# Kernel optimization log

Hardware: AMD Instinct MI355X
Metric: run time of the kernel (lower is better)

Reference implementation:

```python
import jax, jax.numpy as jnp
import numpy as np

B, N, C = 4, 6144, 256
M = 3
n = N // M  # nodes per modality (contiguous blocks)


def setup_inputs() -> dict:
    key = jax.random.key(0)
    ks = jax.random.split(key, 12)
    s = 1.0 / np.sqrt(C)
    sb = 1.0 / np.sqrt(3 * C)
    return {
        "distribution_edge": jax.random.normal(ks[0], (B, N, N), jnp.float32),
        "feature_node": jax.random.normal(ks[1], (B, N, C), jnp.float32),
        "modal_id": jnp.broadcast_to(jnp.repeat(jnp.arange(M, dtype=jnp.int32), n), (B, N)),
        # per-modality params, stacked on leading axis of size M=3
        "W_feat": jax.random.normal(ks[2], (M, C, C), jnp.float32) * s,
        "b_feat": jax.random.normal(ks[3], (M, C), jnp.float32) * s,
        "W_raw": jax.random.normal(ks[4], (M, C, C), jnp.float32) * s,
        "b_raw": jax.random.normal(ks[5], (M, C), jnp.float32) * s,
        "W_beta": jax.random.normal(ks[6], (M, 3 * C), jnp.float32) * sb,
        "b_beta": jax.random.normal(ks[7], (M,), jnp.float32) * sb,
        "ln_gamma": jnp.ones((M, C), jnp.float32),
        "ln_beta": jnp.zeros((M, C), jnp.float32),
    }


def reference(distribution_edge, feature_node, modal_id, W_feat, b_feat,
              W_raw, b_raw, W_beta, b_beta, ln_gamma, ln_beta):
    EPS_L1, EPS_LN = 1e-12, 1e-5  # torch F.normalize / LayerNorm defaults
    diag_mask = 1.0 - jnp.eye(n, dtype=distribution_edge.dtype)  # zero self-edges
    outs = []
    for i in range(M):  # fixed small modality loop (structurally distinct params)
        sl = slice(i * n, (i + 1) * n)
        # masked L1 row-normalization of intra-modality edges  [B,n,n]
        e = distribution_edge[:, sl, sl] * diag_mask
        e = e / jnp.maximum(jnp.sum(jnp.abs(e), axis=-1, keepdims=True), EPS_L1)
        x = feature_node[:, sl, :]  # [B,n,C]
        # neighbor aggregation + linear projections
        aggr = jnp.einsum('bij,bjc->bic', e, x) @ W_raw[i] + b_raw[i]
        feat = x @ W_feat[i] + b_feat[i]
        # sigmoid gate over concatenated features -> [B,n,1]
        cat = jnp.concatenate([feat, aggr, feat - aggr], axis=-1)
        beta = jax.nn.sigmoid(cat @ W_beta[i] + b_beta[i])[..., None]
        h = feat * beta + aggr * (1.0 - beta)
        mu = jnp.mean(h, axis=-1, keepdims=True)
        var = jnp.mean((h - mu) ** 2, axis=-1, keepdims=True)
        h = (h - mu) * jax.lax.rsqrt(var + EPS_LN) * ln_gamma[i] + ln_beta[i]
        outs.append(jax.nn.relu(h))
    return jnp.concatenate(outs, axis=1)  # [B,N,C]
```

## Files before the change

### kernel.cpp

```cpp
#include <hip/hip_runtime.h>
#include <cstdint>
#include <cstddef>

#define B_   4
#define N_   6144
#define C_   256
#define M_   3
#define NLOC 2048

static_assert(N_ == M_ * NLOC, "shape");

typedef __bf16 bf16;
typedef __bf16 bf16x8 __attribute__((ext_vector_type(8)));
typedef float  f32x4  __attribute__((ext_vector_type(4)));

__global__ void transpose_k(const float* __restrict__ src, bf16* __restrict__ dst,
                            int R, int Cc) {
    __shared__ bf16 tile[32][33];
    const int s  = blockIdx.z;
    const int rb = blockIdx.y * 32, cb = blockIdx.x * 32;
    const float* sp = src + (size_t)s * R * Cc;
    bf16*        dp = dst + (size_t)s * R * Cc;
    const int tx = threadIdx.x, ty = threadIdx.y;
#pragma unroll
    for (int i = 0; i < 4; ++i)
        tile[ty + 8 * i][tx] = (bf16)sp[(size_t)(rb + ty + 8 * i) * Cc + (cb + tx)];
    __syncthreads();
#pragma unroll
    for (int i = 0; i < 4; ++i)
        dp[(size_t)(cb + ty + 8 * i) * R + (rb + tx)] = tile[tx][ty + 8 * i];
}

__global__ __launch_bounds__(256) void aggr_gemm_k(
    const float* __restrict__ e,
    const bf16* __restrict__ xT,
    bf16* __restrict__ aggr)
{
    __shared__ __align__(16) bf16 Abuf[64 * 32];
    __shared__ __align__(16) bf16 Bbuf[256 * 32];
    __shared__ float rsum[256];

    const int rt = blockIdx.x, i = blockIdx.y, b = blockIdx.z;
    const int t = threadIdx.x;
    const int w = t >> 6, lane = t & 63, l15 = lane & 15, quad = lane >> 4;

    const int r_stage = t >> 2;
    const int ch8 = (t & 3) * 8;

    const int diag_local = rt * 64 + r_stage;
    const float* eptr = e + ((size_t)(b * N_ + i * NLOC + rt * 64 + r_stage)) * N_
                          + i * NLOC + ch8;
    const bf16* xTbase = xT + (size_t)(b * C_) * N_ + i * NLOC + ch8;

    f32x4 acc[4][4];
#pragma unroll
    for (int mt = 0; mt < 4; ++mt)
#pragma unroll
        for (int nt = 0; nt < 4; ++nt) { f32x4 z = {0.f, 0.f, 0.f, 0.f}; acc[mt][nt] = z; }

    float psum = 0.f;

    for (int kk = 0; kk < NLOC; kk += 32) {
        __syncthreads();
        f32x4 v0 = *(const f32x4*)(const void*)(eptr + kk);
        f32x4 v1 = *(const f32x4*)(const void*)(eptr + kk + 4);
        float vals[8] = {v0[0], v0[1], v0[2], v0[3], v1[0], v1[1], v1[2], v1[3]};
        const int d = diag_local - kk - ch8;
        if ((unsigned)d < 8u) vals[d] = 0.f;
        bf16x8 ab;
#pragma unroll
        for (int j = 0; j < 8; ++j) {
            const bf16 h = (bf16)vals[j];
            ab[j] = h;
            psum += fabsf((float)h);
        }
        *(bf16x8*)(void*)&Abuf[r_stage * 32 + ch8] = ab;
#pragma unroll
        for (int q = 0; q < 4; ++q) {
            const int c = q * 64 + r_stage;
            f32x4 v = *(const f32x4*)(const void*)(xTbase + (size_t)c * N_ + kk);
            *(f32x4*)(void*)&Bbuf[c * 32 + ch8] = v;
        }
        __syncthreads();
        bf16x8 af[4];
#pragma unroll
        for (int mt = 0; mt < 4; ++mt)
            af[mt] = *(const bf16x8*)(const void*)&Abuf[(mt * 16 + l15) * 32 + quad * 8];
#pragma unroll
        for (int nt = 0; nt < 4; ++nt) {
            bf16x8 bv = *(const bf16x8*)(const void*)&Bbuf[(w * 64 + nt * 16 + l15) * 32 + quad * 8];
#pragma unroll
            for (int mt = 0; mt < 4; ++mt)
                acc[mt][nt] = __builtin_amdgcn_mfma_f32_16x16x32_bf16(af[mt], bv, acc[mt][nt], 0, 0, 0);
        }
    }

    rsum[t] = psum;
    __syncthreads();

#pragma unroll
    for (int mt = 0; mt < 4; ++mt) {
#pragma unroll
        for (int reg = 0; reg < 4; ++reg) {
            const int rr = mt * 16 + quad * 4 + reg;
            const float s = rsum[rr * 4] + rsum[rr * 4 + 1] + rsum[rr * 4 + 2] + rsum[rr * 4 + 3];
            const float inv = 1.f / fmaxf(s, 1e-12f);
            bf16* op = aggr + ((size_t)(b * N_ + i * NLOC + rt * 64 + rr)) * C_;
#pragma unroll
            for (int nt = 0; nt < 4; ++nt) {
                const int c = w * 64 + nt * 16 + l15;
                op[c] = (bf16)(acc[mt][nt][reg] * inv);
            }
        }
    }
}

__global__ __launch_bounds__(256) void node_final_k(
    const float* __restrict__ x,
    const bf16* __restrict__ aggr,
    const bf16* __restrict__ WfT,
    const bf16* __restrict__ WrT,
    const float* __restrict__ b_feat,
    const float* __restrict__ b_raw,
    const float* __restrict__ W_beta,
    const float* __restrict__ b_beta,
    const float* __restrict__ ln_g,
    const float* __restrict__ ln_b,
    float* __restrict__ out)
{
    __shared__ __align__(16) bf16 Ax[64 * 32], Ag[64 * 32];
    __shared__ __align__(16) bf16 Bf[256 * 32], Br[256 * 32];
    __shared__ float pbf[256], pbr[256], pwA[256], pwB[256], pgm[256], plb[256];

    const int rt = blockIdx.x, i = blockIdx.y, b = blockIdx.z;
    const int t = threadIdx.x;
    const int w = t >> 6, lane = t & 63, l15 = lane & 15, quad = lane >> 4;

    {
        const int c = t;
        const float w3 = W_beta[i * 768 + 512 + c];
        pbf[c] = b_feat[i * C_ + c];
        pbr[c] = b_raw[i * C_ + c];
        pwA[c] = W_beta[i * 768 + c] + w3;
        pwB[c] = W_beta[i * 768 + 256 + c] - w3;
        pgm[c] = ln_g[i * C_ + c];
        plb[c] = ln_b[i * C_ + c];
    }

    f32x4 accf[16], accg[16];
#pragma unroll
    for (int nt = 0; nt < 16; ++nt) { f32x4 z = {0.f, 0.f, 0.f, 0.f}; accf[nt] = z; accg[nt] = z; }

    const int r_stage = t >> 2;
    const int ch8 = (t & 3) * 8;
    const size_t nodeRow = (size_t)(b * N_ + i * NLOC + rt * 64 + r_stage);
    const float* xp = x   + nodeRow * C_ + ch8;
    const bf16* gp = aggr + nodeRow * C_ + ch8;
    const bf16* wf = WfT + (size_t)(i * C_) * C_ + ch8;
    const bf16* wr = WrT + (size_t)(i * C_) * C_ + ch8;

    for (int kk = 0; kk < C_; kk += 32) {
        __syncthreads();
        {
            f32x4 v0 = *(const f32x4*)(const void*)(xp + kk);
            f32x4 v1 = *(const f32x4*)(const void*)(xp + kk + 4);
            bf16x8 ax;
#pragma unroll
            for (int j = 0; j < 4; ++j) { ax[j] = (bf16)v0[j]; ax[j + 4] = (bf16)v1[j]; }
            *(bf16x8*)(void*)&Ax[r_stage * 32 + ch8] = ax;
        }
        *(f32x4*)(void*)&Ag[r_stage * 32 + ch8] = *(const f32x4*)(const void*)(gp + kk);
#pragma unroll
        for (int q = 0; q < 4; ++q) {
            const int o = q * 64 + r_stage;
            *(f32x4*)(void*)&Bf[o * 32 + ch8] = *(const f32x4*)(const void*)(wf + (size_t)o * C_ + kk);
            *(f32x4*)(void*)&Br[o * 32 + ch8] = *(const f32x4*)(const void*)(wr + (size_t)o * C_ + kk);
        }
        __syncthreads();
        const bf16x8 ax = *(const bf16x8*)(const void*)&Ax[(w * 16 + l15) * 32 + quad * 8];
        const bf16x8 ag = *(const bf16x8*)(const void*)&Ag[(w * 16 + l15) * 32 + quad * 8];
#pragma unroll
        for (int nt = 0; nt < 16; ++nt) {
            const bf16x8 bfv = *(const bf16x8*)(const void*)&Bf[(nt * 16 + l15) * 32 + quad * 8];
            const bf16x8 brv = *(const bf16x8*)(const void*)&Br[(nt * 16 + l15) * 32 + quad * 8];
            accf[nt] = __builtin_amdgcn_mfma_f32_16x16x32_bf16(ax, bfv, accf[nt], 0, 0, 0);
            accg[nt] = __builtin_amdgcn_mfma_f32_16x16x32_bf16(ag, brv, accg[nt], 0, 0, 0);
        }
    }

    const float bb = b_beta[i];
    const int rowbase = i * NLOC + rt * 64 + w * 16 + quad * 4;
#pragma unroll
    for (int reg = 0; reg < 4; ++reg) {
        float pb = 0.f;
#pragma unroll
        for (int nt = 0; nt < 16; ++nt) {
            const int c = nt * 16 + l15;
            const float f = accf[nt][reg] + pbf[c];
            const float g = accg[nt][reg] + pbr[c];
            pb += f * pwA[c] + g * pwB[c];
        }
#pragma unroll
        for (int off = 1; off < 16; off <<= 1) pb += __shfl_xor(pb, off, 16);
        const float beta = 1.f / (1.f + expf(-(pb + bb)));
        float sh = 0.f, sh2 = 0.f;
#pragma unroll
        for (int nt = 0; nt < 16; ++nt) {
            const int c = nt * 16 + l15;
            const float f = accf[nt][reg] + pbf[c];
            const float g = accg[nt][reg] + pbr[c];
            const float h = g + (f - g) * beta;
            sh += h; sh2 += h * h;
        }
#pragma unroll
        for (int off = 1; off < 16; off <<= 1) {
            sh  += __shfl_xor(sh,  off, 16);
            sh2 += __shfl_xor(sh2, off, 16);
        }
        const float mu   = sh * (1.f / 256.f);
        const float var  = sh2 * (1.f / 256.f) - mu * mu;
        const float rstd = rsqrtf(var + 1e-5f);
        float* op = out + (size_t)(b * N_ + rowbase + reg) * C_;
#pragma unroll
        for (int nt = 0; nt < 16; ++nt) {
            const int c = nt * 16 + l15;
            const float f = accf[nt][reg] + pbf[c];
            const float g = accg[nt][reg] + pbr[c];
            const float h = g + (f - g) * beta;
            const float o = (h - mu) * rstd * pgm[c] + plb[c];
            op[c] = fmaxf(o, 0.f);
        }
    }
}

extern "C" void kernel_launch(void* const* d_in, const int* in_sizes, int n_in,
                              void* d_out, int out_size, void* d_ws, size_t ws_size,
                              hipStream_t stream) {
    const float* e       = (const float*)d_in[0];
    const float* x       = (const float*)d_in[1];
    const float* W_feat  = (const float*)d_in[3];
    const float* b_feat  = (const float*)d_in[4];
    const float* W_raw   = (const float*)d_in[5];
    const float* b_raw   = (const float*)d_in[6];
    const float* W_beta  = (const float*)d_in[7];
    const float* b_beta  = (const float*)d_in[8];
    const float* ln_g    = (const float*)d_in[9];
    const float* ln_b    = (const float*)d_in[10];
    float* out = (float*)d_out;

    char* ws = (char*)d_ws;
    bf16* xT   = (bf16*)(ws);
    bf16* WfT  = (bf16*)(ws + 12582912);
    bf16* WrT  = (bf16*)(ws + 12582912 + 393216);
    bf16* aggr = (bf16*)(ws + 12582912 + 2 * 393216);

    dim3 tb(32, 8);
    transpose_k<<<dim3(C_ / 32, N_ / 32, B_), tb, 0, stream>>>(x, xT, N_, C_);
    transpose_k<<<dim3(C_ / 32, C_ / 32, M_), tb, 0, stream>>>(W_feat, WfT, C_, C_);
    transpose_k<<<dim3(C_ / 32, C_ / 32, M_), tb, 0, stream>>>(W_raw, WrT, C_, C_);

    aggr_gemm_k<<<dim3(NLOC / 64, M_, B_), 256, 0, stream>>>(e, xT, aggr);
    node_final_k<<<dim3(NLOC / 64, M_, B_), 256, 0, stream>>>(
        x, aggr, WfT, WrT, b_feat, b_raw, W_beta, b_beta, ln_g, ln_b, out);
}
```

Measured before the change: 814.8 us.

## Fuse aggregation GEMM with node epilogue, double-buffer loads, merge transposes

The three transpose launches become one kernel, and the aggregation GEMM and node-final kernel become a single kernel. The normalised aggregate now stays in LDS instead of going through a bf16 global buffer. The row tile shrinks from 64 to 32, which doubles the number of blocks, and the edge and xT loads are register double-buffered with split barriers. The cost is that each block re-reads the full W_feat and W_raw tiles per 32 rows, and the LayerNorm needs cross-wave reductions through LDS.

```diff
diff --git a/kernel.cpp b/kernel.cpp
--- a/kernel.cpp
+++ b/kernel.cpp
@@ -7,227 +7,329 @@
 #define C_   256
 #define M_   3
 #define NLOC 2048
+#define R_T  32
 
 static_assert(N_ == M_ * NLOC, "shape");
 
 typedef __bf16 bf16;
+typedef __bf16 bf16x4 __attribute__((ext_vector_type(4)));
 typedef __bf16 bf16x8 __attribute__((ext_vector_type(8)));
 typedef float  f32x4  __attribute__((ext_vector_type(4)));
 
-__global__ void transpose_k(const float* __restrict__ src, bf16* __restrict__ dst,
-                            int R, int Cc) {
+#define BARRIER_LGKM() asm volatile("s_waitcnt lgkmcnt(0)\n\ts_barrier" ::: "memory")
+
+__global__ void transpose_all_k(const float* __restrict__ x,
+                                const float* __restrict__ Wf,
+                                const float* __restrict__ Wr,
+                                bf16* __restrict__ xT,
+                                bf16* __restrict__ WfT,
+                                bf16* __restrict__ WrT) {
+    const int id = blockIdx.x;
+    const float* src;
+    bf16* dst;
+    int R, rb, cb;
+    if (id < 6144) {
+        const int s = id / 1536, r = id % 1536;
+        rb = (r >> 3) * 32; cb = (r & 7) * 32;
+        src = x  + (size_t)s * N_ * C_;
+        dst = xT + (size_t)s * N_ * C_;
+        R = N_;
+    } else {
+        const int id2 = id - 6144;
+        const int mat = id2 / 192, r = id2 % 192;
+        const int s = r / 64, r2 = r % 64;
+        rb = (r2 >> 3) * 32; cb = (r2 & 7) * 32;
+        src = (mat ? Wr : Wf) + (size_t)s * C_ * C_;
+        dst = (mat ? WrT : WfT) + (size_t)s * C_ * C_;
+        R = C_;
+    }
     __shared__ bf16 tile[32][33];
-    const int s  = blockIdx.z;
-    const int rb = blockIdx.y * 32, cb = blockIdx.x * 32;
-    const float* sp = src + (size_t)s * R * Cc;
-    bf16*        dp = dst + (size_t)s * R * Cc;
     const int tx = threadIdx.x, ty = threadIdx.y;
 #pragma unroll
-    for (int i = 0; i < 4; ++i)
-        tile[ty + 8 * i][tx] = (bf16)sp[(size_t)(rb + ty + 8 * i) * Cc + (cb + tx)];
-    __syncthreads();
-#pragma unroll
-    for (int i = 0; i < 4; ++i)
-        dp[(size_t)(cb + ty + 8 * i) * R + (rb + tx)] = tile[tx][ty + 8 * i];
+    for (int k = 0; k < 4; ++k)
+        tile[ty + 8 * k][tx] = (bf16)src[(size_t)(rb + ty + 8 * k) * C_ + (cb + tx)];
+    __syncthreads();
+#pragma unroll
+    for (int k = 0; k < 4; ++k)
+        dst[(size_t)(cb + ty + 8 * k) * R + (rb + tx)] = tile[tx][ty + 8 * k];
 }
 
-__global__ __launch_bounds__(256) void aggr_gemm_k(
+struct P1 {
+    bf16  Abuf[2][4][R_T][8];
+    bf16  Bbuf[2][4][256][8];
+    float rsum[R_T][8];
+};
+struct P2 {
+    bf16  Pg[32][R_T][8];
+    bf16  Bw[4][256][8];
+    float prm[6][256];
+    float red[3][2][R_T];
+    float rinv[R_T];
+};
+union FusedLds { P1 p1; P2 p2; };
+
+__global__ __launch_bounds__(256) void fused_k(
     const float* __restrict__ e,
-    const bf16* __restrict__ xT,
-    bf16* __restrict__ aggr)
+    const float* __restrict__ x,
+    const bf16*  __restrict__ xT,
+    const bf16*  __restrict__ WfT,
+    const bf16*  __restrict__ WrT,
+    const float* __restrict__ b_feat, const float* __restrict__ b_raw,
+    const float* __restrict__ W_beta, const float* __restrict__ b_beta,
+    const float* __restrict__ ln_g,   const float* __restrict__ ln_b,
+    float* __restrict__ out)
 {
-    __shared__ __align__(16) bf16 Abuf[64 * 32];
-    __shared__ __align__(16) bf16 Bbuf[256 * 32];
-    __shared__ float rsum[256];
+    __shared__ FusedLds u;
 
     const int rt = blockIdx.x, i = blockIdx.y, b = blockIdx.z;
     const int t = threadIdx.x;
     const int w = t >> 6, lane = t & 63, l15 = lane & 15, quad = lane >> 4;
-
-    const int r_stage = t >> 2;
-    const int ch8 = (t & 3) * 8;
-
-    const int diag_local = rt * 64 + r_stage;
-    const float* eptr = e + ((size_t)(b * N_ + i * NLOC + rt * 64 + r_stage)) * N_
-                          + i * NLOC + ch8;
-    const bf16* xTbase = xT + (size_t)(b * C_) * N_ + i * NLOC + ch8;
-
-    f32x4 acc[4][4];
-#pragma unroll
-    for (int mt = 0; mt < 4; ++mt)
+    const int R0 = rt * R_T;
+
+    const int ar  = t >> 3;
+    const int ac4 = (t & 7) * 4;
+    const int bc  = t >> 2;
+    const int bch8 = (t & 3) * 8;
+    const int dconst = R0 + ar - ac4;
+
+    const float* eptr = e + ((size_t)(b * N_ + i * NLOC + R0 + ar)) * N_
+                          + i * NLOC + ac4;
+    const bf16* xTb = xT + ((size_t)(b * C_ + bc)) * N_ + i * NLOC + bch8;
+
+    f32x4 acc[2][4];
+#pragma unroll
+    for (int mt = 0; mt < 2; ++mt)
 #pragma unroll
         for (int nt = 0; nt < 4; ++nt) { f32x4 z = {0.f, 0.f, 0.f, 0.f}; acc[mt][nt] = z; }
-
     float psum = 0.f;
 
-    for (int kk = 0; kk < NLOC; kk += 32) {
-        __syncthreads();
-        f32x4 v0 = *(const f32x4*)(const void*)(eptr + kk);
-        f32x4 v1 = *(const f32x4*)(const void*)(eptr + kk + 4);
-        float vals[8] = {v0[0], v0[1], v0[2], v0[3], v1[0], v1[1], v1[2], v1[3]};
-        const int d = diag_local - kk - ch8;
-        if ((unsigned)d < 8u) vals[d] = 0.f;
-        bf16x8 ab;
-#pragma unroll
-        for (int j = 0; j < 8; ++j) {
-            const bf16 h = (bf16)vals[j];
-            ab[j] = h;
-            psum += fabsf((float)h);
-        }
-        *(bf16x8*)(void*)&Abuf[r_stage * 32 + ch8] = ab;
-#pragma unroll
-        for (int q = 0; q < 4; ++q) {
-            const int c = q * 64 + r_stage;
-            f32x4 v = *(const f32x4*)(const void*)(xTbase + (size_t)c * N_ + kk);
-            *(f32x4*)(void*)&Bbuf[c * 32 + ch8] = v;
-        }
-        __syncthreads();
-        bf16x8 af[4];
-#pragma unroll
-        for (int mt = 0; mt < 4; ++mt)
-            af[mt] = *(const bf16x8*)(const void*)&Abuf[(mt * 16 + l15) * 32 + quad * 8];
-#pragma unroll
-        for (int nt = 0; nt < 4; ++nt) {
-            bf16x8 bv = *(const bf16x8*)(const void*)&Bbuf[(w * 64 + nt * 16 + l15) * 32 + quad * 8];
-#pragma unroll
-            for (int mt = 0; mt < 4; ++mt)
-                acc[mt][nt] = __builtin_amdgcn_mfma_f32_16x16x32_bf16(af[mt], bv, acc[mt][nt], 0, 0, 0);
-        }
-    }
-
-    rsum[t] = psum;
-    __syncthreads();
-
-#pragma unroll
-    for (int mt = 0; mt < 4; ++mt) {
-#pragma unroll
-        for (int reg = 0; reg < 4; ++reg) {
-            const int rr = mt * 16 + quad * 4 + reg;
-            const float s = rsum[rr * 4] + rsum[rr * 4 + 1] + rsum[rr * 4 + 2] + rsum[rr * 4 + 3];
-            const float inv = 1.f / fmaxf(s, 1e-12f);
-            bf16* op = aggr + ((size_t)(b * N_ + i * NLOC + rt * 64 + rr)) * C_;
-#pragma unroll
-            for (int nt = 0; nt < 4; ++nt) {
-                const int c = w * 64 + nt * 16 + l15;
-                op[c] = (bf16)(acc[mt][nt][reg] * inv);
-            }
-        }
-    }
-}
-
-__global__ __launch_bounds__(256) void node_final_k(
-    const float* __restrict__ x,
-    const bf16* __restrict__ aggr,
-    const bf16* __restrict__ WfT,
-    const bf16* __restrict__ WrT,
-    const float* __restrict__ b_feat,
-    const float* __restrict__ b_raw,
-    const float* __restrict__ W_beta,
-    const float* __restrict__ b_beta,
-    const float* __restrict__ ln_g,
-    const float* __restrict__ ln_b,
-    float* __restrict__ out)
-{
-    __shared__ __align__(16) bf16 Ax[64 * 32], Ag[64 * 32];
-    __shared__ __align__(16) bf16 Bf[256 * 32], Br[256 * 32];
-    __shared__ float pbf[256], pbr[256], pwA[256], pwB[256], pgm[256], plb[256];
-
-    const int rt = blockIdx.x, i = blockIdx.y, b = blockIdx.z;
-    const int t = threadIdx.x;
-    const int w = t >> 6, lane = t & 63, l15 = lane & 15, quad = lane >> 4;
-
+    f32x4 eA, xA0, xA1, xA2, xA3;
+    f32x4 eB, xB0, xB1, xB2, xB3;
+
+#define AG_LOAD(EV, X0, X1, X2, X3, KK)                                          \
+    do {                                                                         \
+        EV = *(const f32x4*)(const void*)(eptr + (KK));                          \
+        X0 = *(const f32x4*)(const void*)(xTb + (size_t)0   * N_ + (KK));        \
+        X1 = *(const f32x4*)(const void*)(xTb + (size_t)64  * N_ + (KK));        \
+        X2 = *(const f32x4*)(const void*)(xTb + (size_t)128 * N_ + (KK));        \
+        X3 = *(const f32x4*)(const void*)(xTb + (size_t)192 * N_ + (KK));        \
+    } while (0)
+
+#define AG_STAGE(EV, X0, X1, X2, X3, KK, BUF)                                    \
+    do {                                                                         \
+        const int d = dconst - (KK);                                             \
+        bf16x4 a4;                                                               \
+        _Pragma("unroll")                                                        \
+        for (int j = 0; j < 4; ++j) {                                            \
+            float v = (EV)[j];                                                   \
+            v = (d == j) ? 0.f : v;                                              \
+            const bf16 hh = (bf16)v;                                             \
+            a4[j] = hh;                                                          \
+            psum += fabsf((float)hh);                                            \
+        }                                                                        \
+        *(bf16x4*)(void*)&u.p1.Abuf[BUF][ac4 >> 3][ar][ac4 & 7] = a4;            \
+        *(f32x4*)(void*)&u.p1.Bbuf[BUF][t & 3][bc      ][0] = X0;                \
+        *(f32x4*)(void*)&u.p1.Bbuf[BUF][t & 3][bc +  64][0] = X1;                \
+        *(f32x4*)(void*)&u.p1.Bbuf[BUF][t & 3][bc + 128][0] = X2;                \
+        *(f32x4*)(void*)&u.p1.Bbuf[BUF][t & 3][bc + 192][0] = X3;                \
+    } while (0)
+
+#define AG_COMPUTE(BUF)                                                          \
+    do {                                                                         \
+        const bf16x8 af0 = *(const bf16x8*)(const void*)&u.p1.Abuf[BUF][quad][l15][0];      \
+        const bf16x8 af1 = *(const bf16x8*)(const void*)&u.p1.Abuf[BUF][quad][16 + l15][0]; \
+        _Pragma("unroll")                                                        \
+        for (int nt = 0; nt < 4; ++nt) {                                         \
+            const bf16x8 bv = *(const bf16x8*)(const void*)                      \
+                &u.p1.Bbuf[BUF][quad][w * 64 + nt * 16 + l15][0];                \
+            acc[0][nt] = __builtin_amdgcn_mfma_f32_16x16x32_bf16(af0, bv, acc[0][nt], 0, 0, 0); \
+            acc[1][nt] = __builtin_amdgcn_mfma_f32_16x16x32_bf16(af1, bv, acc[1][nt], 0, 0, 0); \
+        }                                                                        \
+    } while (0)
+
+    AG_LOAD(eA, xA0, xA1, xA2, xA3, 0);
+#pragma unroll 1
+    for (int kk = 0; kk < NLOC; kk += 64) {
+        AG_LOAD(eB, xB0, xB1, xB2, xB3, kk + 32);
+        AG_STAGE(eA, xA0, xA1, xA2, xA3, kk, 0);
+        BARRIER_LGKM();
+        if (kk + 64 < NLOC) AG_LOAD(eA, xA0, xA1, xA2, xA3, kk + 64);
+        AG_COMPUTE(0);
+        AG_STAGE(eB, xB0, xB1, xB2, xB3, kk + 32, 1);
+        BARRIER_LGKM();
+        AG_COMPUTE(1);
+    }
+#undef AG_LOAD
+#undef AG_STAGE
+#undef AG_COMPUTE
+
+    u.p1.rsum[ar][t & 7] = psum;
+    __syncthreads();
+    float rs = 0.f;
+    if (t < R_T) {
+#pragma unroll
+        for (int j = 0; j < 8; ++j) rs += u.p1.rsum[t][j];
+    }
+    __syncthreads();
+    if (t < R_T) u.p2.rinv[t] = 1.f / fmaxf(rs, 1e-12f);
     {
         const int c = t;
         const float w3 = W_beta[i * 768 + 512 + c];
-        pbf[c] = b_feat[i * C_ + c];
-        pbr[c] = b_raw[i * C_ + c];
-        pwA[c] = W_beta[i * 768 + c] + w3;
-        pwB[c] = W_beta[i * 768 + 256 + c] - w3;
-        pgm[c] = ln_g[i * C_ + c];
-        plb[c] = ln_b[i * C_ + c];
-    }
-
-    f32x4 accf[16], accg[16];
-#pragma unroll
-    for (int nt = 0; nt < 16; ++nt) { f32x4 z = {0.f, 0.f, 0.f, 0.f}; accf[nt] = z; accg[nt] = z; }
-
-    const int r_stage = t >> 2;
-    const int ch8 = (t & 3) * 8;
-    const size_t nodeRow = (size_t)(b * N_ + i * NLOC + rt * 64 + r_stage);
-    const float* xp = x   + nodeRow * C_ + ch8;
-    const bf16* gp = aggr + nodeRow * C_ + ch8;
-    const bf16* wf = WfT + (size_t)(i * C_) * C_ + ch8;
-    const bf16* wr = WrT + (size_t)(i * C_) * C_ + ch8;
-
+        u.p2.prm[0][c] = b_feat[i * C_ + c];
+        u.p2.prm[1][c] = b_raw[i * C_ + c];
+        u.p2.prm[2][c] = W_beta[i * 768 + c] + w3;
+        u.p2.prm[3][c] = W_beta[i * 768 + 256 + c] - w3;
+        u.p2.prm[4][c] = ln_g[i * C_ + c];
+        u.p2.prm[5][c] = ln_b[i * C_ + c];
+    }
+    __syncthreads();
+#pragma unroll
+    for (int mt = 0; mt < 2; ++mt) {
+#pragma unroll
+        for (int reg = 0; reg < 4; ++reg) {
+            const int r = mt * 16 + quad * 4 + reg;
+            const float iv = u.p2.rinv[r];
+#pragma unroll
+            for (int nt = 0; nt < 4; ++nt) {
+                const int c = w * 64 + nt * 16 + l15;
+                u.p2.Pg[c >> 3][r][c & 7] = (bf16)(acc[mt][nt][reg] * iv);
+            }
+        }
+    }
+    __syncthreads();
+
+    const int rg = w & 1, cg = w >> 1;
+    const int wo = t >> 2;
+    const int wch8 = (t & 3) * 8;
+
+    const float* xrowp = x + ((size_t)(b * N_ + i * NLOC + R0 + rg * 16 + l15)) * C_ + quad * 8;
+    const bf16* wfp = WfT + ((size_t)(i * C_ + wo)) * C_ + wch8;
+    const bf16* wrp = WrT + ((size_t)(i * C_ + wo)) * C_ + wch8;
+
+    f32x4 accf[8], accg[8];
+#pragma unroll
+    for (int nt = 0; nt < 8; ++nt) { f32x4 z = {0.f, 0.f, 0.f, 0.f}; accf[nt] = z; accg[nt] = z; }
+
+    f32x4 wv0, wv1, wv2, wv3, xv0, xv1;
+
+#define NF_LOADW(P, KK)                                                          \
+    do {                                                                         \
+        wv0 = *(const f32x4*)(const void*)((P) + (size_t)0   * C_ + (KK));       \
+        wv1 = *(const f32x4*)(const void*)((P) + (size_t)64  * C_ + (KK));       \
+        wv2 = *(const f32x4*)(const void*)((P) + (size_t)128 * C_ + (KK));       \
+        wv3 = *(const f32x4*)(const void*)((P) + (size_t)192 * C_ + (KK));       \
+    } while (0)
+
+#define NF_STOREW()                                                              \
+    do {                                                                         \
+        *(f32x4*)(void*)&u.p2.Bw[t & 3][wo      ][0] = wv0;                      \
+        *(f32x4*)(void*)&u.p2.Bw[t & 3][wo +  64][0] = wv1;                      \
+        *(f32x4*)(void*)&u.p2.Bw[t & 3][wo + 128][0] = wv2;                      \
+        *(f32x4*)(void*)&u.p2.Bw[t & 3][wo + 192][0] = wv3;                      \
+    } while (0)
+
+    NF_LOADW(wfp, 0);
+    xv0 = *(const f32x4*)(const void*)(xrowp);
+    xv1 = *(const f32x4*)(const void*)(xrowp + 4);
+#pragma unroll 1
     for (int kk = 0; kk < C_; kk += 32) {
-        __syncthreads();
-        {
-            f32x4 v0 = *(const f32x4*)(const void*)(xp + kk);
-            f32x4 v1 = *(const f32x4*)(const void*)(xp + kk + 4);
-            bf16x8 ax;
-#pragma unroll
-            for (int j = 0; j < 4; ++j) { ax[j] = (bf16)v0[j]; ax[j + 4] = (bf16)v1[j]; }
-            *(bf16x8*)(void*)&Ax[r_stage * 32 + ch8] = ax;
-        }
-        *(f32x4*)(void*)&Ag[r_stage * 32 + ch8] = *(const f32x4*)(const void*)(gp + kk);
-#pragma unroll
-        for (int q = 0; q < 4; ++q) {
-            const int o = q * 64 + r_stage;
-            *(f32x4*)(void*)&Bf[o * 32 + ch8] = *(const f32x4*)(const void*)(wf + (size_t)o * C_ + kk);
-            *(f32x4*)(void*)&Br[o * 32 + ch8] = *(const f32x4*)(const void*)(wr + (size_t)o * C_ + kk);
-        }
-        __syncthreads();
-        const bf16x8 ax = *(const bf16x8*)(const void*)&Ax[(w * 16 + l15) * 32 + quad * 8];
-        const bf16x8 ag = *(const bf16x8*)(const void*)&Ag[(w * 16 + l15) * 32 + quad * 8];
-#pragma unroll
-        for (int nt = 0; nt < 16; ++nt) {
-            const bf16x8 bfv = *(const bf16x8*)(const void*)&Bf[(nt * 16 + l15) * 32 + quad * 8];
-            const bf16x8 brv = *(const bf16x8*)(const void*)&Br[(nt * 16 + l15) * 32 + quad * 8];
-            accf[nt] = __builtin_amdgcn_mfma_f32_16x16x32_bf16(ax, bfv, accf[nt], 0, 0, 0);
-            accg[nt] = __builtin_amdgcn_mfma_f32_16x16x32_bf16(ag, brv, accg[nt], 0, 0, 0);
-        }
-    }
+        BARRIER_LGKM();
+        NF_STOREW();
+        bf16x8 ax;
+#pragma unroll
+        for (int j = 0; j < 4; ++j) { ax[j] = (bf16)xv0[j]; ax[j + 4] = (bf16)xv1[j]; }
+        if (kk + 32 < C_) {
+            NF_LOADW(wfp, kk + 32);
+            xv0 = *(const f32x4*)(const void*)(xrowp + kk + 32);
+            xv1 = *(const f32x4*)(const void*)(xrowp + kk + 36);
+        }
+        BARRIER_LGKM();
+#pragma unroll
+        for (int nt = 0; nt < 8; ++nt) {
+            const bf16x8 bv = *(const bf16x8*)(const void*)
+                &u.p2.Bw[quad][cg * 128 + nt * 16 + l15][0];
+            accf[nt] = __builtin_amdgcn_mfma_f32_16x16x32_bf16(ax, bv, accf[nt], 0, 0, 0);
+        }
+    }
+
+    NF_LOADW(wrp, 0);
+#pragma unroll 1
+    for (int kk = 0; kk < C_; kk += 32) {
+        BARRIER_LGKM();
+        NF_STOREW();
+        if (kk + 32 < C_) NF_LOADW(wrp, kk + 32);
+        const bf16x8 ag = *(const bf16x8*)(const void*)
+            &u.p2.Pg[(kk >> 3) + quad][rg * 16 + l15][0];
+        BARRIER_LGKM();
+#pragma unroll
+        for (int nt = 0; nt < 8; ++nt) {
+            const bf16x8 bv = *(const bf16x8*)(const void*)
+                &u.p2.Bw[quad][cg * 128 + nt * 16 + l15][0];
+            accg[nt] = __builtin_amdgcn_mfma_f32_16x16x32_bf16(ag, bv, accg[nt], 0, 0, 0);
+        }
+    }
+#undef NF_LOADW
+#undef NF_STOREW
 
     const float bb = b_beta[i];
-    const int rowbase = i * NLOC + rt * 64 + w * 16 + quad * 4;
+    const int rbase = rg * 16 + quad * 4;
+
 #pragma unroll
     for (int reg = 0; reg < 4; ++reg) {
         float pb = 0.f;
 #pragma unroll
-        for (int nt = 0; nt < 16; ++nt) {
-            const int c = nt * 16 + l15;
-            const float f = accf[nt][reg] + pbf[c];
-            const float g = accg[nt][reg] + pbr[c];
-            pb += f * pwA[c] + g * pwB[c];
+        for (int nt = 0; nt < 8; ++nt) {
+            const int c = cg * 128 + nt * 16 + l15;
+            const float f = accf[nt][reg] + u.p2.prm[0][c];
+            const float g = accg[nt][reg] + u.p2.prm[1][c];
+            pb += f * u.p2.prm[2][c] + g * u.p2.prm[3][c];
         }
 #pragma unroll
         for (int off = 1; off < 16; off <<= 1) pb += __shfl_xor(pb, off, 16);
-        const float beta = 1.f / (1.f + expf(-(pb + bb)));
+        if (l15 == 0) u.p2.red[0][cg][rbase + reg] = pb;
+    }
+    __syncthreads();
+    float beta_r[4];
+#pragma unroll
+    for (int reg = 0; reg < 4; ++reg) {
+        const int r = rbase + reg;
+        const float logit = u.p2.red[0][0][r] + u.p2.red[0][1][r] + bb;
+        const float beta = 1.f / (1.f + expf(-logit));
+        beta_r[reg] = beta;
         float sh = 0.f, sh2 = 0.f;
 #pragma unroll
-        for (int nt = 0; nt < 16; ++nt) {
-            const int c = nt * 16 + l15;
-            const float f = accf[nt][reg] + pbf[c];
-            const float g = accg[nt][reg] + pbr[c];
-            const float h = g + (f - g) * beta;
-            sh += h; sh2 += h * h;
+        for (int nt = 0; nt < 8; ++nt) {
+            const int c = cg * 128 + nt * 16 + l15;
+            const float f = accf[nt][reg] + u.p2.prm[0][c];
+            const float g = accg[nt][reg] + u.p2.prm[1][c];
+            const float hh = g + (f - g) * beta;
+            sh += hh; sh2 += hh * hh;
         }
 #pragma unroll
         for (int off = 1; off < 16; off <<= 1) {
             sh  += __shfl_xor(sh,  off, 16);
             sh2 += __shfl_xor(sh2, off, 16);
         }
+        if (l15 == 0) { u.p2.red[1][cg][r] = sh; u.p2.red[2][cg][r] = sh2; }
+    }
+    __syncthreads();
+#pragma unroll
+    for (int reg = 0; reg < 4; ++reg) {
+        const int r = rbase + reg;
+        const float sh  = u.p2.red[1][0][r] + u.p2.red[1][1][r];
+        const float sh2 = u.p2.red[2][0][r] + u.p2.red[2][1][r];
         const float mu   = sh * (1.f / 256.f);
         const float var  = sh2 * (1.f / 256.f) - mu * mu;
         const float rstd = rsqrtf(var + 1e-5f);
-        float* op = out + (size_t)(b * N_ + rowbase + reg) * C_;
-#pragma unroll
-        for (int nt = 0; nt < 16; ++nt) {
-            const int c = nt * 16 + l15;
-            const float f = accf[nt][reg] + pbf[c];
-            const float g = accg[nt][reg] + pbr[c];
-            const float h = g + (f - g) * beta;
-            const float o = (h - mu) * rstd * pgm[c] + plb[c];
+        const float beta = beta_r[reg];
+        float* op = out + ((size_t)(b * N_ + i * NLOC + R0 + r)) * C_;
+#pragma unroll
+        for (int nt = 0; nt < 8; ++nt) {
+            const int c = cg * 128 + nt * 16 + l15;
+            const float f = accf[nt][reg] + u.p2.prm[0][c];
+            const float g = accg[nt][reg] + u.p2.prm[1][c];
+            const float hh = g + (f - g) * beta;
+            const float o = (hh - mu) * rstd * u.p2.prm[4][c] + u.p2.prm[5][c];
             op[c] = fmaxf(o, 0.f);
         }
     }
@@ -249,17 +351,11 @@
     float* out = (float*)d_out;
 
     char* ws = (char*)d_ws;
-    bf16* xT   = (bf16*)(ws);
-    bf16* WfT  = (bf16*)(ws + 12582912);
-    bf16* WrT  = (bf16*)(ws + 12582912 + 393216);
-    bf16* aggr = (bf16*)(ws + 12582912 + 2 * 393216);
-
-    dim3 tb(32, 8);
-    transpose_k<<<dim3(C_ / 32, N_ / 32, B_), tb, 0, stream>>>(x, xT, N_, C_);
-    transpose_k<<<dim3(C_ / 32, C_ / 32, M_), tb, 0, stream>>>(W_feat, WfT, C_, C_);
-    transpose_k<<<dim3(C_ / 32, C_ / 32, M_), tb, 0, stream>>>(W_raw, WrT, C_, C_);
-
-    aggr_gemm_k<<<dim3(NLOC / 64, M_, B_), 256, 0, stream>>>(e, xT, aggr);
-    node_final_k<<<dim3(NLOC / 64, M_, B_), 256, 0, stream>>>(
-        x, aggr, WfT, WrT, b_feat, b_raw, W_beta, b_beta, ln_g, ln_b, out);
+    bf16* xT  = (bf16*)(ws);
+    bf16* WfT = (bf16*)(ws + 12582912);
+    bf16* WrT = (bf16*)(ws + 12582912 + 393216);
+
+    transpose_all_k<<<6528, dim3(32, 8), 0, stream>>>(x, W_feat, W_raw, xT, WfT, WrT);
+    fused_k<<<dim3(NLOC / R_T, M_, B_), 256, 0, stream>>>(
+        e, x, xT, WfT, WrT, b_feat, b_raw, W_beta, b_beta, ln_g, ln_b, out);
 }
```

Result: slower. 834.0 us (+2.4%).
